# Optimization experiments

Measured on AMD Instinct MI355X. Metric: run time of the kernel, lower is better.

Reference implementation:

```python
import jax, jax.numpy as jnp
import numpy as np
import math

B, N, SEEDS, DIM, H = 16, 2048, 4, 512, 8
DS = DIM // H
EPS = 1e-5
LOG_2PI = math.log(2.0 * math.pi)


def setup_inputs() -> dict:
    key = jax.random.key(0)
    ks = jax.random.split(key, 12)
    s = 1.0 / math.sqrt(DIM)
    d = {}
    d["X"] = jax.random.normal(ks[0], (B, N, SEEDS, DIM), jnp.float32)
    # seed parameters (kaiming/xavier-ish init)
    d["M"] = jax.random.uniform(ks[1], (1, SEEDS, DIM), jnp.float32, -s, s) * math.sqrt(6.0)
    d["S"] = jax.random.uniform(ks[2], (1, SEEDS, DIM), jnp.float32, -s, s) * math.sqrt(6.0)
    d["p"] = jax.random.uniform(ks[3], (1, SEEDS), jnp.float32, -0.5, 0.5)
    # linear layers (PyTorch Linear: y = x @ W.T + b)
    d["Wk"] = jax.random.uniform(ks[4], (DIM, DIM), jnp.float32, -s, s)
    d["bk"] = jax.random.uniform(ks[5], (DIM,), jnp.float32, -s, s)
    d["Wv"] = jax.random.uniform(ks[6], (DIM, DIM), jnp.float32, -s, s)
    d["bv"] = jax.random.uniform(ks[7], (DIM,), jnp.float32, -s, s)
    d["Wo"] = jax.random.uniform(ks[8], (DIM, DIM), jnp.float32, -s, s)
    d["bo"] = jax.random.uniform(ks[9], (DIM,), jnp.float32, -s, s)
    # batchnorm affine params (init: weight=1, bias=0)
    d["g0"] = jnp.ones((SEEDS * DIM,), jnp.float32)
    d["b0"] = jnp.zeros((SEEDS * DIM,), jnp.float32)
    d["g1"] = jnp.ones((SEEDS * DIM,), jnp.float32)
    d["b1"] = jnp.zeros((SEEDS * DIM,), jnp.float32)
    return d


def _batchnorm(x, g, b):
    # BatchNorm1d in training mode: batch stats (biased variance), eps=1e-5
    m = x.mean(axis=0)
    v = x.var(axis=0)
    return g * (x - m) / jnp.sqrt(v + EPS) + b


def reference(X, M, S, p, Wk, bk, Wv, bv, Wo, bo, g0, b0, g1, b1):
    mu = M[0].reshape(SEEDS, H, DS)                      # [S,H,DS] per-head seeds
    sigma = jax.nn.softplus(S[0]).reshape(SEEDS, H, DS)  # [S,H,DS]
    logp = jnp.log(jax.nn.softmax(p[0], axis=-1))        # [S]

    K = (X @ Wk.T + bk).reshape(B, N, SEEDS, H, DS)
    V = (X @ Wv.T + bv).reshape(B, N, SEEDS, H, DS)

    # GMM log-likelihood scores: sum over per-head feature dim
    diff = K - mu                                        # [B,N,S,H,DS]
    ll = (-0.5 * LOG_2PI - jnp.log(sigma) - 0.5 * diff * diff / (sigma * sigma)).sum(-1)
    ll = ll + logp[:, None]                              # [B,N,S,H]

    A = jax.nn.softmax(ll / math.sqrt(DIM), axis=1)      # softmax over instances n
    O = mu + jnp.einsum('bnsh,bnshd->bshd', A, V)        # [B,S,H,DS]
    O = O.reshape(B, SEEDS, DIM)                         # head-major feature concat

    O = _batchnorm(O.reshape(B, SEEDS * DIM), g0, b0).reshape(B, SEEDS, DIM)
    O = O + jax.nn.relu(O @ Wo.T + bo)
    O = _batchnorm(O.reshape(B, SEEDS * DIM), g1, b1).reshape(B, SEEDS, DIM)
    return O
```

## Files before the change

kernel.cpp:

```cpp
#include <hip/hip_runtime.h>
#include <hip/hip_bf16.h>

typedef __attribute__((ext_vector_type(4))) float f32x4;
typedef __attribute__((ext_vector_type(8))) short bf16x8;

constexpr int NB = 16, NN = 2048, NS = 4, NDIM = 512, NH = 8, NDS = 64;
constexpr float LOG2PI = 1.8378770664093453f;
constexpr float INV_SQRT_DIM = 0.04419417382415922f;

__device__ inline short f2bf(float f) {
  __hip_bfloat16 h = __float2bfloat16(f);
  return *reinterpret_cast<short*>(&h);
}
__device__ inline float bf2f(short b) {
  union { unsigned u; float f; } v;
  v.u = ((unsigned)(unsigned short)b) << 16;
  return v.f;
}

__device__ inline void gld16(const void* g, void* l) {
  __builtin_amdgcn_global_load_lds(
      (const __attribute__((address_space(1))) void*)g,
      (__attribute__((address_space(3))) void*)l, 16, 0, 0);
}

__global__ __launch_bounds__(256) void cvtx_kernel(
    const float* __restrict__ in, short* __restrict__ out, int n8)
{
  const int stride = gridDim.x * blockDim.x;
  for (int i = blockIdx.x * blockDim.x + threadIdx.x; i < n8; i += stride) {
    const float4 a = reinterpret_cast<const float4*>(in)[(size_t)i * 2];
    const float4 b = reinterpret_cast<const float4*>(in)[(size_t)i * 2 + 1];
    bf16x8 o;
    o[0] = f2bf(a.x); o[1] = f2bf(a.y); o[2] = f2bf(a.z); o[3] = f2bf(a.w);
    o[4] = f2bf(b.x); o[5] = f2bf(b.y); o[6] = f2bf(b.z); o[7] = f2bf(b.w);
    *reinterpret_cast<bf16x8*>(&out[(size_t)i * 8]) = o;
  }
}

__global__ __launch_bounds__(256) void wvt_kernel(
    const float* __restrict__ Wv, float* __restrict__ WvT)
{
  const int idx = blockIdx.x * 256 + threadIdx.x;
  const int d = idx & 63;
  const int i = (idx >> 6) & 511;
  const int h = idx >> 15;
  WvT[idx] = Wv[(size_t)(h * 64 + d) * 512 + i];
}

__global__ __launch_bounds__(256) void gmmtab_kernel(
    const float* __restrict__ Mp, const float* __restrict__ Sp,
    const float* __restrict__ pp, const float* __restrict__ bkp,
    float4* __restrict__ gmm, float* __restrict__ lp2)
{
  const int idx = blockIdx.x * 256 + threadIdx.x;
  const int Jg = idx & 511;
  const float sv = Sp[idx];
  const float sig = log1pf(expf(sv));
  float4 o;
  o.x = Mp[idx];
  o.y = (-0.5f * LOG2PI - logf(sig)) * INV_SQRT_DIM;
  o.z = (0.5f / (sig * sig)) * INV_SQRT_DIM;
  o.w = bkp[Jg];
  gmm[idx] = o;
  if (idx < 4) {
    const float p0 = pp[0], p1 = pp[1], p2 = pp[2], p3 = pp[3];
    const float pmx = fmaxf(fmaxf(p0, p1), fmaxf(p2, p3));
    const float lse = pmx + logf(expf(p0 - pmx) + expf(p1 - pmx) +
                                 expf(p2 - pmx) + expf(p3 - pmx));
    lp2[idx] = (pp[idx] - lse) * INV_SQRT_DIM;
  }
}

__global__ __launch_bounds__(256) void kproj_kernel(
    const short* __restrict__ Xb, const short* __restrict__ Wkb,
    const float4* __restrict__ gmm, const float* __restrict__ lp2,
    float* __restrict__ ll_ws)
{
  __shared__ short As[2][128 * 32];
  __shared__ short Bs[2][128 * 32];

  const int bid0 = blockIdx.x;
  const int bid = (bid0 & 7) * 512 + (bid0 >> 3);
  const int ct = bid & 3;
  const int mt = bid >> 2;
  const int m0 = mt * 128;
  const int c0 = ct * 128;

  const int t = threadIdx.x;
  const int l = t & 63;
  const int w = t >> 6;
  const int wr = w >> 1, wc = w & 1;
  const int lg = l >> 4, lr = l & 15;

  f32x4 acc[4][4] = {};

  const int sr = l >> 2;
  const int scg = (l & 3) ^ ((l >> 3) & 3);
  const int q1 = 16 * NDIM;
  const int d0 = (w * 32) * 32;
  const int d1 = (w * 32 + 16) * 32;
  const size_t gxa = (size_t)(m0 + w * 32 + sr) * NDIM + scg * 8;
  const size_t gba = (size_t)(c0 + w * 32 + sr) * NDIM + scg * 8;

  auto stage = [&](int buf, int ts) {
    const int k0 = ts << 5;
    gld16(&Xb[gxa + k0],       (char*)&As[buf][d0]);
    gld16(&Xb[gxa + q1 + k0],  (char*)&As[buf][d1]);
    gld16(&Wkb[gba + k0],      (char*)&Bs[buf][d0]);
    gld16(&Wkb[gba + q1 + k0], (char*)&Bs[buf][d1]);
  };

  const int rb = lr * 64 + ((lg ^ ((lr >> 1) & 3)) << 4);

  auto compute = [&](int buf) {
    bf16x8 a[4], b[4];
    const char* Ab = (const char*)&As[buf][0] + rb;
    const char* Bb = (const char*)&Bs[buf][0] + rb;
    #pragma unroll
    for (int i = 0; i < 4; ++i)
      a[i] = *reinterpret_cast<const bf16x8*>(Ab + (wr * 64 + i * 16) * 64);
    #pragma unroll
    for (int j = 0; j < 4; ++j)
      b[j] = *reinterpret_cast<const bf16x8*>(Bb + (wc * 64 + j * 16) * 64);
    #pragma unroll
    for (int i = 0; i < 4; ++i) {
      #pragma unroll
      for (int j = 0; j < 4; ++j)
        acc[i][j] = __builtin_amdgcn_mfma_f32_16x16x32_bf16(a[i], b[j], acc[i][j], 0, 0, 0);
    }
  };

  stage(0, 0);
  __builtin_amdgcn_sched_barrier(0);
  for (int ts = 0; ts < 15; ++ts) {
    stage((ts + 1) & 1, ts + 1);
    asm volatile("s_waitcnt vmcnt(4)" ::: "memory");
    __builtin_amdgcn_s_barrier();
    compute(ts & 1);
    __builtin_amdgcn_s_barrier();
  }
  asm volatile("s_waitcnt vmcnt(0)" ::: "memory");
  __builtin_amdgcn_s_barrier();
  compute(1);
  __builtin_amdgcn_sched_barrier(0);


  const float l0 = lp2[0], l1 = lp2[1], l2 = lp2[2], l3 = lp2[3];
  const float lpv[4] = {l0, l1, l2, l3};

  float part[4][4];
  #pragma unroll
  for (int i = 0; i < 4; ++i)
    #pragma unroll
    for (int e = 0; e < 4; ++e) part[i][e] = 0.f;

  #pragma unroll
  for (int j = 0; j < 4; ++j) {
    const int Jg = c0 + wc * 64 + j * 16 + lr;
    #pragma unroll
    for (int e = 0; e < 4; ++e) {
      const float4 gw = gmm[e * NDIM + Jg];
      #pragma unroll
      for (int i = 0; i < 4; ++i) {
        const float kv = acc[i][j][e] + gw.w;
        const float d = kv - gw.x;
        part[i][e] += gw.y - d * d * gw.z;
      }
    }
  }
  #pragma unroll
  for (int off = 1; off < 16; off <<= 1) {
    #pragma unroll
    for (int i = 0; i < 4; ++i)
      #pragma unroll
      for (int e = 0; e < 4; ++e)
        part[i][e] += __shfl_xor(part[i][e], off, 64);
  }
  if (lr == 0) {
    const int h = ct * 2 + wc;
    #pragma unroll
    for (int i = 0; i < 4; ++i) {
      #pragma unroll
      for (int e = 0; e < 4; ++e) {
        const int R = m0 + wr * 64 + i * 16 + 4 * lg + e;
        const int bn = R >> 2;
        const int bb = bn >> 11;
        const int nn = bn & (NN - 1);
        ll_ws[((size_t)((bb * NS + e) * NH + h)) * NN + nn] = part[i][e] + lpv[e];
      }
    }
  }
}

__global__ __launch_bounds__(256) void stats_kernel(
    const float* __restrict__ ll_ws, float* __restrict__ mxs,
    float* __restrict__ rsum)
{
  __shared__ float sred[8];
  const int g = blockIdx.x;
  const int t = threadIdx.x;
  const int w = t >> 6, l = t & 63;
  const float* ll = ll_ws + (size_t)g * NN;

  float v8[8];
  float mx = -1e30f;
  #pragma unroll
  for (int i = 0; i < 8; ++i) { v8[i] = ll[t + i * 256]; mx = fmaxf(mx, v8[i]); }
  #pragma unroll
  for (int off = 1; off < 64; off <<= 1) mx = fmaxf(mx, __shfl_xor(mx, off, 64));
  if (l == 0) sred[w] = mx;
  __syncthreads();
  mx = fmaxf(fmaxf(sred[0], sred[1]), fmaxf(sred[2], sred[3]));

  float sum = 0.f;
  #pragma unroll
  for (int i = 0; i < 8; ++i) sum += expf(v8[i] - mx);
  #pragma unroll
  for (int off = 1; off < 64; off <<= 1) sum += __shfl_xor(sum, off, 64);
  __syncthreads();
  if (l == 0) sred[4 + w] = sum;
  __syncthreads();
  if (t == 0) {
    mxs[g] = mx;
    rsum[g] = 1.f / (sred[4] + sred[5] + sred[6] + sred[7]);
  }
}

__global__ __launch_bounds__(256) void y_kernel(
    const float* __restrict__ ll_ws, const short* __restrict__ Xb,
    const float* __restrict__ mxs, const float* __restrict__ rsum,
    float* __restrict__ Yp)
{
  __shared__ float wT[256][8];
  const int blk = blockIdx.x;
  const int bs = blk & 63;
  const int nq = blk >> 6;
  const int b = bs >> 2, s = bs & 3;
  const int g0 = bs * 8;
  const int t = threadIdx.x;

  #pragma unroll
  for (int h = 0; h < 8; ++h) {
    const float lv = ll_ws[(size_t)(g0 + h) * NN + nq * 256 + t];
    wT[t][h] = expf(lv - mxs[g0 + h]) * rsum[g0 + h];
  }
  __syncthreads();

  const ushort2* X2 = reinterpret_cast<const ushort2*>(Xb);
  const size_t xbase = ((size_t)(b * 2048 + nq * 256) * 4 + s) * 256 + t;
  float acc[8][2] = {};
  #pragma unroll 4
  for (int n = 0; n < 256; ++n) {
    const ushort2 xv = X2[xbase + (size_t)n * 1024];
    const float x0 = bf2f((short)xv.x), x1 = bf2f((short)xv.y);
    const float4 w0 = *reinterpret_cast<const float4*>(&wT[n][0]);
    const float4 w1 = *reinterpret_cast<const float4*>(&wT[n][4]);
    acc[0][0] += w0.x * x0; acc[0][1] += w0.x * x1;
    acc[1][0] += w0.y * x0; acc[1][1] += w0.y * x1;
    acc[2][0] += w0.z * x0; acc[2][1] += w0.z * x1;
    acc[3][0] += w0.w * x0; acc[3][1] += w0.w * x1;
    acc[4][0] += w1.x * x0; acc[4][1] += w1.x * x1;
    acc[5][0] += w1.y * x0; acc[5][1] += w1.y * x1;
    acc[6][0] += w1.z * x0; acc[6][1] += w1.z * x1;
    acc[7][0] += w1.w * x0; acc[7][1] += w1.w * x1;
  }
  #pragma unroll
  for (int h = 0; h < 8; ++h) {
    float* yp = Yp + ((size_t)((nq * 64 + bs) * 8 + h)) * 512 + 2 * t;
    yp[0] = acc[h][0]; yp[1] = acc[h][1];
  }
}

__global__ __launch_bounds__(256) void poolproj_kernel(
    const float* __restrict__ Yp, const float* __restrict__ WvT,
    const float* __restrict__ bvp, const float* __restrict__ Mp,
    float* __restrict__ O0)
{
  __shared__ float ys[512];
  __shared__ float pr[4][64];
  const int g = blockIdx.x;
  const int bs = g >> 3, h = g & 7;
  const int s = bs & 3;
  const int t = threadIdx.x;

  float a0 = 0.f, a1 = 0.f;
  #pragma unroll
  for (int q = 0; q < 8; ++q) {
    const float* yp = Yp + ((size_t)((q * 64 + bs) * 8 + h)) * 512;
    a0 += yp[t];
    a1 += yp[t + 256];
  }
  ys[t] = a0; ys[t + 256] = a1;
  __syncthreads();

  const int d = t & 63, p = t >> 6;
  const float* wt = WvT + ((size_t)h * 512 + p * 128) * 64 + d;
  const float* yy = ys + p * 128;
  float acc = 0.f;
  #pragma unroll 4
  for (int i = 0; i < 128; ++i) acc += yy[i] * wt[(size_t)i * 64];
  pr[p][d] = acc;
  __syncthreads();
  if (t < 64) {
    const float tot = pr[0][t] + pr[1][t] + pr[2][t] + pr[3][t];
    O0[(size_t)g * 64 + t] = Mp[s * NDIM + h * NDS + t] + bvp[h * 64 + t] + tot;
  }
}

__global__ __launch_bounds__(256) void bn_kernel(
    const float* __restrict__ Xin, const float* __restrict__ gg,
    const float* __restrict__ bb, float* __restrict__ Yo)
{
  const int f = blockIdx.x * 256 + threadIdx.x;
  float x[NB];
  float m = 0.f;
  #pragma unroll
  for (int b = 0; b < NB; ++b) { x[b] = Xin[b * (NS * NDIM) + f]; m += x[b]; }
  m *= (1.f / NB);
  float v = 0.f;
  #pragma unroll
  for (int b = 0; b < NB; ++b) { const float d = x[b] - m; v += d * d; }
  v *= (1.f / NB);
  const float inv = rsqrtf(v + 1e-5f) * gg[f];
  const float bf = bb[f];
  #pragma unroll
  for (int b = 0; b < NB; ++b) Yo[b * (NS * NDIM) + f] = (x[b] - m) * inv + bf;
}

__global__ __launch_bounds__(256) void mlp_kernel(
    const float* __restrict__ Yi, const float* __restrict__ Wo,
    const float* __restrict__ bo, float* __restrict__ Zo)
{
  const int idx = blockIdx.x * 256 + threadIdx.x;
  const int r = idx >> 9, j = idx & 511;
  const float4* yr = reinterpret_cast<const float4*>(Yi + (size_t)r * NDIM);
  const float4* wrow = reinterpret_cast<const float4*>(Wo + (size_t)j * NDIM);
  float acc = 0.f;
  #pragma unroll 4
  for (int i = 0; i < NDIM / 4; ++i) {
    const float4 a = yr[i], b = wrow[i];
    acc += a.x * b.x + a.y * b.y + a.z * b.z + a.w * b.w;
  }
  const float rl = acc + bo[j];
  Zo[idx] = Yi[idx] + fmaxf(rl, 0.f);
}

extern "C" void kernel_launch(void* const* d_in, const int* in_sizes, int n_in,
                              void* d_out, int out_size, void* d_ws, size_t ws_size,
                              hipStream_t stream) {
  (void)in_sizes; (void)n_in; (void)out_size; (void)ws_size;
  const float* X  = (const float*)d_in[0];
  const float* M  = (const float*)d_in[1];
  const float* S  = (const float*)d_in[2];
  const float* p  = (const float*)d_in[3];
  const float* Wk = (const float*)d_in[4];
  const float* bk = (const float*)d_in[5];
  const float* Wv = (const float*)d_in[6];
  const float* bv = (const float*)d_in[7];
  const float* Wo = (const float*)d_in[8];
  const float* bo = (const float*)d_in[9];
  const float* g0 = (const float*)d_in[10];
  const float* b0 = (const float*)d_in[11];
  const float* g1 = (const float*)d_in[12];
  const float* b1 = (const float*)d_in[13];

  char* ws = (char*)d_ws;
  short* Xb    = (short*)ws;
  float* ll_ws = (float*)(ws + (size_t)134217728);
  float* mxs   = (float*)(ws + (size_t)138412032);
  float* rsum  = (float*)(ws + (size_t)138414080);
  float* Yp    = (float*)(ws + (size_t)138416128);
  float* O0    = (float*)(ws + (size_t)146804736);
  float* Y     = (float*)(ws + (size_t)146935808);
  float* Z     = (float*)(ws + (size_t)147066880);
  short* Wkb   = (short*)(ws + (size_t)147197952);
  float* WvT   = (float*)(ws + (size_t)147722240);
  float4* gmm  = (float4*)(ws + (size_t)148770816);
  float* lp2   = (float*)(ws + (size_t)148803584);

  cvtx_kernel<<<128, 256, 0, stream>>>(Wk, Wkb, 32768);
  wvt_kernel<<<1024, 256, 0, stream>>>(Wv, WvT);
  gmmtab_kernel<<<8, 256, 0, stream>>>(M, S, p, bk, gmm, lp2);
  cvtx_kernel<<<2048, 256, 0, stream>>>(X, Xb, 8388608);
  kproj_kernel<<<4096, 256, 0, stream>>>(Xb, Wkb, gmm, lp2, ll_ws);
  stats_kernel<<<512, 256, 0, stream>>>(ll_ws, mxs, rsum);
  y_kernel<<<512, 256, 0, stream>>>(ll_ws, Xb, mxs, rsum, Yp);
  poolproj_kernel<<<512, 256, 0, stream>>>(Yp, WvT, bv, M, O0);
  bn_kernel<<<8, 256, 0, stream>>>(O0, g0, b0, Y);
  mlp_kernel<<<128, 256, 0, stream>>>(Y, Wo, bo, Z);
  bn_kernel<<<8, 256, 0, stream>>>(Z, g1, b1, (float*)d_out);
}
```

Measured before the change: 270.3 us.

## Double K-tile depth in K-projection GEMM and merge weight-prep kernels

The bf16 MFMA K-projection GEMM now stages 64-wide K slices instead of 32. This halves the number of loop iterations and barriers, and uses a new 8-group XOR swizzle for the LDS layout. LDS use per block doubles to 64 KB, which may reduce occupancy. Three small preparation kernels (Wv transpose, Wk bf16 conversion, GMM table) are also merged into one launch to cut launch overhead.

After: 257.7 us. 4.7% less time.

```diff
diff --git a/kernel.cpp b/kernel.cpp
--- a/kernel.cpp
+++ b/kernel.cpp
@@ -38,37 +38,47 @@
   }
 }
 
-__global__ __launch_bounds__(256) void wvt_kernel(
-    const float* __restrict__ Wv, float* __restrict__ WvT)
-{
-  const int idx = blockIdx.x * 256 + threadIdx.x;
-  const int d = idx & 63;
-  const int i = (idx >> 6) & 511;
-  const int h = idx >> 15;
-  WvT[idx] = Wv[(size_t)(h * 64 + d) * 512 + i];
-}
-
-__global__ __launch_bounds__(256) void gmmtab_kernel(
+__global__ __launch_bounds__(256) void prep_kernel(
+    const float* __restrict__ Wv, float* __restrict__ WvT,
+    const float* __restrict__ Wk, short* __restrict__ Wkb,
     const float* __restrict__ Mp, const float* __restrict__ Sp,
     const float* __restrict__ pp, const float* __restrict__ bkp,
     float4* __restrict__ gmm, float* __restrict__ lp2)
 {
-  const int idx = blockIdx.x * 256 + threadIdx.x;
-  const int Jg = idx & 511;
-  const float sv = Sp[idx];
-  const float sig = log1pf(expf(sv));
-  float4 o;
-  o.x = Mp[idx];
-  o.y = (-0.5f * LOG2PI - logf(sig)) * INV_SQRT_DIM;
-  o.z = (0.5f / (sig * sig)) * INV_SQRT_DIM;
-  o.w = bkp[Jg];
-  gmm[idx] = o;
-  if (idx < 4) {
-    const float p0 = pp[0], p1 = pp[1], p2 = pp[2], p3 = pp[3];
-    const float pmx = fmaxf(fmaxf(p0, p1), fmaxf(p2, p3));
-    const float lse = pmx + logf(expf(p0 - pmx) + expf(p1 - pmx) +
-                                 expf(p2 - pmx) + expf(p3 - pmx));
-    lp2[idx] = (pp[idx] - lse) * INV_SQRT_DIM;
+  const int blk = blockIdx.x;
+  const int tid = threadIdx.x;
+  if (blk < 1024) {
+    const int idx = blk * 256 + tid;
+    const int d = idx & 63;
+    const int i = (idx >> 6) & 511;
+    const int h = idx >> 15;
+    WvT[idx] = Wv[(size_t)(h * 64 + d) * 512 + i];
+  } else if (blk < 1152) {
+    const int j = (blk - 1024) * 256 + tid;
+    const float4 a = reinterpret_cast<const float4*>(Wk)[(size_t)j * 2];
+    const float4 b = reinterpret_cast<const float4*>(Wk)[(size_t)j * 2 + 1];
+    bf16x8 o;
+    o[0] = f2bf(a.x); o[1] = f2bf(a.y); o[2] = f2bf(a.z); o[3] = f2bf(a.w);
+    o[4] = f2bf(b.x); o[5] = f2bf(b.y); o[6] = f2bf(b.z); o[7] = f2bf(b.w);
+    *reinterpret_cast<bf16x8*>(&Wkb[(size_t)j * 8]) = o;
+  } else {
+    const int idx = (blk - 1152) * 256 + tid;
+    const int Jg = idx & 511;
+    const float sv = Sp[idx];
+    const float sig = log1pf(expf(sv));
+    float4 o;
+    o.x = Mp[idx];
+    o.y = (-0.5f * LOG2PI - logf(sig)) * INV_SQRT_DIM;
+    o.z = (0.5f / (sig * sig)) * INV_SQRT_DIM;
+    o.w = bkp[Jg];
+    gmm[idx] = o;
+    if (idx < 4) {
+      const float p0 = pp[0], p1 = pp[1], p2 = pp[2], p3 = pp[3];
+      const float pmx = fmaxf(fmaxf(p0, p1), fmaxf(p2, p3));
+      const float lse = pmx + logf(expf(p0 - pmx) + expf(p1 - pmx) +
+                                   expf(p2 - pmx) + expf(p3 - pmx));
+      lp2[idx] = (pp[idx] - lse) * INV_SQRT_DIM;
+    }
   }
 }
 
@@ -77,8 +87,8 @@
     const float4* __restrict__ gmm, const float* __restrict__ lp2,
     float* __restrict__ ll_ws)
 {
-  __shared__ short As[2][128 * 32];
-  __shared__ short Bs[2][128 * 32];
+  __shared__ short As[2][128 * 64];
+  __shared__ short Bs[2][128 * 64];
 
   const int bid0 = blockIdx.x;
   const int bid = (bid0 & 7) * 512 + (bid0 >> 3);
@@ -95,47 +105,52 @@
 
   f32x4 acc[4][4] = {};
 
-  const int sr = l >> 2;
-  const int scg = (l & 3) ^ ((l >> 3) & 3);
-  const int q1 = 16 * NDIM;
-  const int d0 = (w * 32) * 32;
-  const int d1 = (w * 32 + 16) * 32;
-  const size_t gxa = (size_t)(m0 + w * 32 + sr) * NDIM + scg * 8;
-  const size_t gba = (size_t)(c0 + w * 32 + sr) * NDIM + scg * 8;
+  const int g8 = (l & 7) ^ (l >> 3);
+  const size_t gxa = (size_t)(m0 + w * 32 + (l >> 3)) * NDIM + g8 * 8;
+  const size_t gba = (size_t)(c0 + w * 32 + (l >> 3)) * NDIM + g8 * 8;
+  const int dA = (w * 32) * 64;
 
   auto stage = [&](int buf, int ts) {
-    const int k0 = ts << 5;
-    gld16(&Xb[gxa + k0],       (char*)&As[buf][d0]);
-    gld16(&Xb[gxa + q1 + k0],  (char*)&As[buf][d1]);
-    gld16(&Wkb[gba + k0],      (char*)&Bs[buf][d0]);
-    gld16(&Wkb[gba + q1 + k0], (char*)&Bs[buf][d1]);
-  };
-
-  const int rb = lr * 64 + ((lg ^ ((lr >> 1) & 3)) << 4);
-
-  auto compute = [&](int buf) {
-    bf16x8 a[4], b[4];
-    const char* Ab = (const char*)&As[buf][0] + rb;
-    const char* Bb = (const char*)&Bs[buf][0] + rb;
-    #pragma unroll
-    for (int i = 0; i < 4; ++i)
-      a[i] = *reinterpret_cast<const bf16x8*>(Ab + (wr * 64 + i * 16) * 64);
-    #pragma unroll
-    for (int j = 0; j < 4; ++j)
-      b[j] = *reinterpret_cast<const bf16x8*>(Bb + (wc * 64 + j * 16) * 64);
-    #pragma unroll
-    for (int i = 0; i < 4; ++i) {
-      #pragma unroll
-      for (int j = 0; j < 4; ++j)
-        acc[i][j] = __builtin_amdgcn_mfma_f32_16x16x32_bf16(a[i], b[j], acc[i][j], 0, 0, 0);
+    const int k0 = ts << 6;
+    #pragma unroll
+    for (int q = 0; q < 4; ++q) {
+      const size_t so = (size_t)(q * 8) * NDIM + k0;
+      const int dd = dA + (q * 8) * 64;
+      gld16(&Xb[gxa + so],  (char*)&As[buf][dd]);
+      gld16(&Wkb[gba + so], (char*)&Bs[buf][dd]);
     }
   };
 
+  auto compute = [&](int buf) {
+    #pragma unroll
+    for (int kk = 0; kk < 64; kk += 32) {
+      bf16x8 a[4], b[4];
+      #pragma unroll
+      for (int i = 0; i < 4; ++i) {
+        const int r = wr * 64 + i * 16 + lr;
+        const int byte = r * 128 + ((((kk >> 3) + lg) ^ (lr & 7)) << 4);
+        a[i] = *reinterpret_cast<const bf16x8*>((const char*)&As[buf][0] + byte);
+      }
+      #pragma unroll
+      for (int j = 0; j < 4; ++j) {
+        const int r = wc * 64 + j * 16 + lr;
+        const int byte = r * 128 + ((((kk >> 3) + lg) ^ (lr & 7)) << 4);
+        b[j] = *reinterpret_cast<const bf16x8*>((const char*)&Bs[buf][0] + byte);
+      }
+      #pragma unroll
+      for (int i = 0; i < 4; ++i) {
+        #pragma unroll
+        for (int j = 0; j < 4; ++j)
+          acc[i][j] = __builtin_amdgcn_mfma_f32_16x16x32_bf16(a[i], b[j], acc[i][j], 0, 0, 0);
+      }
+    }
+  };
+
   stage(0, 0);
   __builtin_amdgcn_sched_barrier(0);
-  for (int ts = 0; ts < 15; ++ts) {
+  for (int ts = 0; ts < 7; ++ts) {
     stage((ts + 1) & 1, ts + 1);
-    asm volatile("s_waitcnt vmcnt(4)" ::: "memory");
+    asm volatile("s_waitcnt vmcnt(8)" ::: "memory");
     __builtin_amdgcn_s_barrier();
     compute(ts & 1);
     __builtin_amdgcn_s_barrier();
@@ -379,9 +394,7 @@
   float4* gmm  = (float4*)(ws + (size_t)148770816);
   float* lp2   = (float*)(ws + (size_t)148803584);
 
-  cvtx_kernel<<<128, 256, 0, stream>>>(Wk, Wkb, 32768);
-  wvt_kernel<<<1024, 256, 0, stream>>>(Wv, WvT);
-  gmmtab_kernel<<<8, 256, 0, stream>>>(M, S, p, bk, gmm, lp2);
+  prep_kernel<<<1160, 256, 0, stream>>>(Wv, WvT, Wk, Wkb, M, S, p, bk, gmm, lp2);
   cvtx_kernel<<<2048, 256, 0, stream>>>(X, Xb, 8388608);
   kproj_kernel<<<4096, 256, 0, stream>>>(Xb, Wkb, gmm, lp2, ll_ws);
   stats_kernel<<<512, 256, 0, stream>>>(ll_ws, mxs, rsum);
```
